# Kernel tuning notes

Hardware: AMD Instinct MI355X
Metric: run time of the kernel (lower is better)

The kernel has to match this reference:

```python
import jax, jax.numpy as jnp
import numpy as np

INTERVAL = 0.5  # voxel_size_ratio
N_RAYS = 131072
M_SAMPLES = 8388608  # ~64 samples per ray on average
ALPHA_INIT = 0.01


def setup_inputs() -> dict:
    key = jax.random.key(0)
    k1, k2, k3 = jax.random.split(key, 3)
    density = jax.random.normal(k1, (M_SAMPLES,), jnp.float32)
    rgb_feat = jax.random.normal(k2, (M_SAMPLES, 3), jnp.float32)  # raw k0 colors
    # act_shift buffer: log(1/(1-alpha_init) - 1)
    shift = jnp.array([np.log(1.0 / (1.0 - ALPHA_INIT) - 1.0)], jnp.float32)
    # sorted ray ids (samples along each ray are contiguous, near->far)
    ray_id = jnp.sort(jax.random.randint(k3, (M_SAMPLES,), 0, N_RAYS)).astype(jnp.int32)
    return {"density": density, "rgb_feat": rgb_feat, "shift": shift,
            "ray_id": ray_id, "N": N_RAYS}


def reference(density, rgb_feat, shift, ray_id, N):
    # Raw2Alpha: alpha = 1 - (1 + exp(density + shift))^(-interval)
    #          = 1 - exp(-softplus(density + shift) * interval)
    sp = jax.nn.softplus(density + shift[0])
    log1ma = -sp * INTERVAL            # log(1 - alpha), exact
    alpha = 1.0 - jnp.exp(log1ma)

    # Alphas2Weights: per-ray exclusive cumulative product of (1 - alpha)
    # done in log space with a segmented exclusive cumsum.
    seg_tot = jax.ops.segment_sum(log1ma, ray_id, num_segments=N)   # [N] log prod per ray
    seg_excl = jnp.cumsum(seg_tot) - seg_tot                        # log prod of previous rays
    within_excl = jnp.cumsum(log1ma) - log1ma - seg_excl[ray_id]    # exclusive within segment
    T = jnp.exp(within_excl)          # transmittance before each sample
    weights = alpha * T               # [M]
    alphainv_last = jnp.exp(seg_tot)  # [N] leftover transmittance per ray

    # composite colors per ray + white-ish background via alphainv_last
    rgb = jax.nn.sigmoid(rgb_feat)
    rgb_marched = jax.ops.segment_sum(weights[:, None] * rgb, ray_id, num_segments=N)
    out = rgb_marched + alphainv_last[:, None]   # [N, 3]
    return weights, alphainv_last, out
```

## Files before the change

kernel.cpp:

```cpp
#include <hip/hip_runtime.h>


__device__ __forceinline__ float fast_sigmoid(float x) {
    return __builtin_amdgcn_rcpf(1.0f + __expf(-x));
}

#define DPP_ADD(x, ctrl, rmask)                                               \
    do {                                                                      \
        int _s = __builtin_amdgcn_update_dpp(0, __float_as_int(x), (ctrl),    \
                                             (rmask), 0xf, true);             \
        (x) += __int_as_float(_s);                                            \
    } while (0)

#define DPP_MUL(x, ctrl, rmask)                                               \
    do {                                                                      \
        int _s = __builtin_amdgcn_update_dpp(0x3f800000, __float_as_int(x),   \
                                             (ctrl), (rmask), 0xf, false);    \
        (x) *= __int_as_float(_s);                                            \
    } while (0)

__device__ __forceinline__ float wave_scan_add(float x) {
    DPP_ADD(x, 0x111, 0xf);
    DPP_ADD(x, 0x112, 0xf);
    DPP_ADD(x, 0x114, 0xf);
    DPP_ADD(x, 0x118, 0xf);
    DPP_ADD(x, 0x142, 0xa);
    DPP_ADD(x, 0x143, 0xc);
    return x;
}

__device__ __forceinline__ float wave_scan_mul(float x) {
    DPP_MUL(x, 0x111, 0xf);
    DPP_MUL(x, 0x112, 0xf);
    DPP_MUL(x, 0x114, 0xf);
    DPP_MUL(x, 0x118, 0xf);
    DPP_MUL(x, 0x142, 0xa);
    DPP_MUL(x, 0x143, 0xc);
    return x;
}

__device__ __forceinline__ float bcast_lane63(float x) {
    return __int_as_float(__builtin_amdgcn_readlane(__float_as_int(x), 63));
}

__global__ __launch_bounds__(256) void seg_starts4_kernel(
    const int4* __restrict__ ray4, int M4, int M, int N,
    const int* __restrict__ ray_id, int* __restrict__ starts)
{
    const int i = blockIdx.x * blockDim.x + threadIdx.x;
    if (i >= M4) return;
    const int4 v = ray4[i];
    const int prev = (i == 0) ? -1 : ray_id[4 * i - 1];
    const int base = 4 * i;
    for (int r = prev + 1; r <= v.x; ++r) starts[r] = base;
    for (int r = v.x + 1;  r <= v.y; ++r) starts[r] = base + 1;
    for (int r = v.y + 1;  r <= v.z; ++r) starts[r] = base + 2;
    for (int r = v.z + 1;  r <= v.w; ++r) starts[r] = base + 3;
    if (i == M4 - 1) {
        int last = v.w;
        for (int j = 4 * M4; j < M; ++j) {
            const int cur = ray_id[j];
            for (int r = last + 1; r <= cur; ++r) starts[r] = j;
            last = cur;
        }
        for (int r = last + 1; r <= N; ++r) starts[r] = M;
    }
}

#define RPW 4

__global__ __launch_bounds__(256) void favor_render_kernel(
    const float* __restrict__ density,
    const float* __restrict__ rgb_feat,
    const float* __restrict__ shift,
    const int*   __restrict__ starts,
    int M, int N,
    float* __restrict__ weights,
    float* __restrict__ alphainv_last,
    float* __restrict__ out3)
{
    const int wave = (blockIdx.x * blockDim.x + threadIdx.x) >> 6;
    const int t    = threadIdx.x & 63;
    const int r0   = wave * RPW;
    if (r0 >= N) return;

    const int bv = starts[min(r0 + t, N)];
    int s[RPW + 1];
    #pragma unroll
    for (int k = 0; k <= RPW; ++k)
        s[k] = __builtin_amdgcn_readlane(bv, k);

    const float sh = shift[0];

    float pd[RPW], pr[RPW], pg[RPW], pb[RPW];
    #pragma unroll
    for (int j = 0; j < RPW; ++j) {
        const int c = max(min(s[j] + t, s[j + 1] - 1), 0);
        pd[j] = density[c];
        pr[j] = rgb_feat[3 * c + 0];
        pg[j] = rgb_feat[3 * c + 1];
        pb[j] = rgb_feat[3 * c + 2];
    }

    #pragma unroll
    for (int j = 0; j < RPW; ++j) {
        const int ray = r0 + j;
        if (ray >= N) continue;
        const int st = s[j], en = s[j + 1];

        float carryT = 1.0f;
        float a0 = 0.0f, a1 = 0.0f, a2 = 0.0f;

        {
            const bool valid = (st + t) < en;
            const float u = 1.0f + __expf(pd[j] + sh);
            const float a = __builtin_amdgcn_rsqf(u);
            const float m = valid ? a : 1.0f;
            const float S = wave_scan_mul(m);
            const float tot = bcast_lane63(S);
            const float w = S * (u * a - 1.0f);
            if (valid) {
                weights[st + t] = w;
                a0 = w * fast_sigmoid(pr[j]);
                a1 = w * fast_sigmoid(pg[j]);
                a2 = w * fast_sigmoid(pb[j]);
            }
            carryT = tot;
        }

        for (int base = st + 64; base < en; base += 64) {
            const int i = base + t;
            const bool valid = i < en;
            const int c = min(i, en - 1);
            const float d = density[c];
            const float r = rgb_feat[3 * c + 0];
            const float g = rgb_feat[3 * c + 1];
            const float b = rgb_feat[3 * c + 2];
            const float u = 1.0f + __expf(d + sh);
            const float a = __builtin_amdgcn_rsqf(u);
            const float m = valid ? a : 1.0f;
            const float S = wave_scan_mul(m);
            const float tot = bcast_lane63(S);
            const float w = carryT * S * (u * a - 1.0f);
            if (valid) {
                weights[i] = w;
                a0 += w * fast_sigmoid(r);
                a1 += w * fast_sigmoid(g);
                a2 += w * fast_sigmoid(b);
            }
            carryT *= tot;
        }

        const float t0 = bcast_lane63(wave_scan_add(a0));
        const float t1 = bcast_lane63(wave_scan_add(a1));
        const float t2 = bcast_lane63(wave_scan_add(a2));
        if (t == 0) {
            alphainv_last[ray] = carryT;
            out3[3 * ray + 0] = t0 + carryT;
            out3[3 * ray + 1] = t1 + carryT;
            out3[3 * ray + 2] = t2 + carryT;
        }
    }
}

extern "C" void kernel_launch(void* const* d_in, const int* in_sizes, int n_in,
                              void* d_out, int out_size, void* d_ws, size_t ws_size,
                              hipStream_t stream) {
    const float* density  = (const float*)d_in[0];
    const float* rgb_feat = (const float*)d_in[1];
    const float* shift    = (const float*)d_in[2];
    const int*   ray_id   = (const int*)d_in[3];

    const int M = in_sizes[0];
    const int N = (out_size - M) / 4;

    float* weights       = (float*)d_out;
    float* alphainv_last = weights + M;
    float* out3          = alphainv_last + N;

    const int block = 256;
    int* starts = (int*)d_ws;

    const int M4 = M >> 2;
    const int grid_starts = (M4 + block - 1) / block;
    seg_starts4_kernel<<<grid_starts, block, 0, stream>>>(
        (const int4*)ray_id, M4, M, N, ray_id, starts);

    const int n_waves = (N + RPW - 1) / RPW;
    const int grid_render = (n_waves * 64 + block - 1) / block;
    favor_render_kernel<<<grid_render, block, 0, stream>>>(
        density, rgb_feat, shift, starts, M, N,
        weights, alphainv_last, out3);
}
```

Baseline: 215.6 us.

## Prefetch first two 64-sample chunks for all rays and interleave per-ray scans

The render kernel now loads the first two 64-sample chunks of all four rays up front and processes chunk 0 and chunk 1 for every ray in interleaved loops. The final wave reductions are batched across rays, and launch bounds now request 4 blocks per CU. With about 64 samples per ray, most rays fit in these two chunks, so more independent memory loads are in flight before the serial scan work starts. The cost is roughly double the register use for prefetched values, and the occupancy hint may force spills or cap registers.

```diff
diff --git a/kernel.cpp b/kernel.cpp
--- a/kernel.cpp
+++ b/kernel.cpp
@@ -69,7 +69,7 @@
 
 #define RPW 4
 
-__global__ __launch_bounds__(256) void favor_render_kernel(
+__global__ __launch_bounds__(256, 4) void favor_render_kernel(
     const float* __restrict__ density,
     const float* __restrict__ rgb_feat,
     const float* __restrict__ shift,
@@ -92,43 +92,63 @@
 
     const float sh = shift[0];
 
-    float pd[RPW], pr[RPW], pg[RPW], pb[RPW];
-    #pragma unroll
-    for (int j = 0; j < RPW; ++j) {
-        const int c = max(min(s[j] + t, s[j + 1] - 1), 0);
-        pd[j] = density[c];
-        pr[j] = rgb_feat[3 * c + 0];
-        pg[j] = rgb_feat[3 * c + 1];
-        pb[j] = rgb_feat[3 * c + 2];
-    }
-
-    #pragma unroll
-    for (int j = 0; j < RPW; ++j) {
-        const int ray = r0 + j;
-        if (ray >= N) continue;
-        const int st = s[j], en = s[j + 1];
-
-        float carryT = 1.0f;
-        float a0 = 0.0f, a1 = 0.0f, a2 = 0.0f;
-
-        {
-            const bool valid = (st + t) < en;
-            const float u = 1.0f + __expf(pd[j] + sh);
-            const float a = __builtin_amdgcn_rsqf(u);
-            const float m = valid ? a : 1.0f;
-            const float S = wave_scan_mul(m);
-            const float tot = bcast_lane63(S);
-            const float w = S * (u * a - 1.0f);
-            if (valid) {
-                weights[st + t] = w;
-                a0 = w * fast_sigmoid(pr[j]);
-                a1 = w * fast_sigmoid(pg[j]);
-                a2 = w * fast_sigmoid(pb[j]);
-            }
-            carryT = tot;
-        }
-
-        for (int base = st + 64; base < en; base += 64) {
+    float d0[RPW], r0v[RPW], g0v[RPW], b0v[RPW];
+    float d1[RPW], r1v[RPW], g1v[RPW], b1v[RPW];
+    #pragma unroll
+    for (int j = 0; j < RPW; ++j) {
+        const int st = s[j], en = s[j + 1];
+        const int c0 = max(min(st + t,      en - 1), 0);
+        const int c1 = max(min(st + 64 + t, en - 1), 0);
+        d0[j]  = density[c0];
+        r0v[j] = rgb_feat[3 * c0 + 0];
+        g0v[j] = rgb_feat[3 * c0 + 1];
+        b0v[j] = rgb_feat[3 * c0 + 2];
+        d1[j]  = density[c1];
+        r1v[j] = rgb_feat[3 * c1 + 0];
+        g1v[j] = rgb_feat[3 * c1 + 1];
+        b1v[j] = rgb_feat[3 * c1 + 2];
+    }
+
+    float carryT[RPW], accR[RPW], accG[RPW], accB[RPW];
+
+    #pragma unroll
+    for (int j = 0; j < RPW; ++j) {
+        const int st = s[j], en = s[j + 1];
+        const bool valid = (st + t) < en;
+        const float u = 1.0f + __expf(d0[j] + sh);
+        const float a = __builtin_amdgcn_rsqf(u);
+        const float m = valid ? a : 1.0f;
+        const float S = wave_scan_mul(m);
+        carryT[j] = bcast_lane63(S);
+        const float w = S * (u * a - 1.0f);
+        accR[j] = valid ? w * fast_sigmoid(r0v[j]) : 0.0f;
+        accG[j] = valid ? w * fast_sigmoid(g0v[j]) : 0.0f;
+        accB[j] = valid ? w * fast_sigmoid(b0v[j]) : 0.0f;
+        if (valid) weights[st + t] = w;
+    }
+
+    #pragma unroll
+    for (int j = 0; j < RPW; ++j) {
+        const int st = s[j], en = s[j + 1];
+        const int i = st + 64 + t;
+        const bool valid = i < en;
+        const float u = 1.0f + __expf(d1[j] + sh);
+        const float a = __builtin_amdgcn_rsqf(u);
+        const float m = valid ? a : 1.0f;
+        const float S = wave_scan_mul(m);
+        const float tot = bcast_lane63(S);
+        const float w = carryT[j] * S * (u * a - 1.0f);
+        accR[j] += valid ? w * fast_sigmoid(r1v[j]) : 0.0f;
+        accG[j] += valid ? w * fast_sigmoid(g1v[j]) : 0.0f;
+        accB[j] += valid ? w * fast_sigmoid(b1v[j]) : 0.0f;
+        if (valid) weights[i] = w;
+        carryT[j] *= tot;
+    }
+
+    #pragma unroll
+    for (int j = 0; j < RPW; ++j) {
+        const int st = s[j], en = s[j + 1];
+        for (int base = st + 128; base < en; base += 64) {
             const int i = base + t;
             const bool valid = i < en;
             const int c = min(i, en - 1);
@@ -141,24 +161,35 @@
             const float m = valid ? a : 1.0f;
             const float S = wave_scan_mul(m);
             const float tot = bcast_lane63(S);
-            const float w = carryT * S * (u * a - 1.0f);
+            const float w = carryT[j] * S * (u * a - 1.0f);
             if (valid) {
                 weights[i] = w;
-                a0 += w * fast_sigmoid(r);
-                a1 += w * fast_sigmoid(g);
-                a2 += w * fast_sigmoid(b);
+                accR[j] += w * fast_sigmoid(r);
+                accG[j] += w * fast_sigmoid(g);
+                accB[j] += w * fast_sigmoid(b);
             }
-            carryT *= tot;
+            carryT[j] *= tot;
         }
-
-        const float t0 = bcast_lane63(wave_scan_add(a0));
-        const float t1 = bcast_lane63(wave_scan_add(a1));
-        const float t2 = bcast_lane63(wave_scan_add(a2));
-        if (t == 0) {
-            alphainv_last[ray] = carryT;
-            out3[3 * ray + 0] = t0 + carryT;
-            out3[3 * ray + 1] = t1 + carryT;
-            out3[3 * ray + 2] = t2 + carryT;
+    }
+
+    float tR[RPW], tG[RPW], tB[RPW];
+    #pragma unroll
+    for (int j = 0; j < RPW; ++j) {
+        tR[j] = wave_scan_add(accR[j]);
+        tG[j] = wave_scan_add(accG[j]);
+        tB[j] = wave_scan_add(accB[j]);
+    }
+    #pragma unroll
+    for (int j = 0; j < RPW; ++j) {
+        const float sR = bcast_lane63(tR[j]);
+        const float sG = bcast_lane63(tG[j]);
+        const float sB = bcast_lane63(tB[j]);
+        const int ray = r0 + j;
+        if (t == 0 && ray < N) {
+            alphainv_last[ray] = carryT[j];
+            out3[3 * ray + 0] = sR + carryT[j];
+            out3[3 * ray + 1] = sG + carryT[j];
+            out3[3 * ray + 2] = sB + carryT[j];
         }
     }
 }
```

After: 209.9 us. 2.6% less time.

## Split each wave into two half-wave rays, processing four samples per lane

Applied to the files above, without the earlier changes.

The render kernel now assigns one ray to each 32-lane half of a wave (two rays per wave) instead of looping a full wave over four rays. Each lane handles four consecutive samples with vectorized 4-wide loads of density and rgb, takes a local product, and runs a 32-lane DPP scan whose results are redistributed with ds_bpermute. The intent is to cut wasted lanes on short rays (about 64 samples each) and to reduce scan and load instruction overhead per sample. In exchange it adds unaligned vector loads, tail-case branches and a per-lane serial product, and the two halves of a wave now share one loop trip count.

```diff
diff --git a/kernel.cpp b/kernel.cpp
--- a/kernel.cpp
+++ b/kernel.cpp
@@ -4,6 +4,9 @@
 __device__ __forceinline__ float fast_sigmoid(float x) {
     return __builtin_amdgcn_rcpf(1.0f + __expf(-x));
 }
+
+struct __align__(4) f3  { float x, y, z; };
+struct __align__(4) f4s { float x, y, z, w; };
 
 #define DPP_ADD(x, ctrl, rmask)                                               \
     do {                                                                      \
@@ -19,28 +22,26 @@
         (x) *= __int_as_float(_s);                                            \
     } while (0)
 
-__device__ __forceinline__ float wave_scan_add(float x) {
+__device__ __forceinline__ float half_scan_mul(float x) {
+    DPP_MUL(x, 0x111, 0xf);
+    DPP_MUL(x, 0x112, 0xf);
+    DPP_MUL(x, 0x114, 0xf);
+    DPP_MUL(x, 0x118, 0xf);
+    DPP_MUL(x, 0x142, 0xa);
+    return x;
+}
+__device__ __forceinline__ float half_scan_add(float x) {
     DPP_ADD(x, 0x111, 0xf);
     DPP_ADD(x, 0x112, 0xf);
     DPP_ADD(x, 0x114, 0xf);
     DPP_ADD(x, 0x118, 0xf);
     DPP_ADD(x, 0x142, 0xa);
-    DPP_ADD(x, 0x143, 0xc);
     return x;
 }
 
-__device__ __forceinline__ float wave_scan_mul(float x) {
-    DPP_MUL(x, 0x111, 0xf);
-    DPP_MUL(x, 0x112, 0xf);
-    DPP_MUL(x, 0x114, 0xf);
-    DPP_MUL(x, 0x118, 0xf);
-    DPP_MUL(x, 0x142, 0xa);
-    DPP_MUL(x, 0x143, 0xc);
-    return x;
-}
-
-__device__ __forceinline__ float bcast_lane63(float x) {
-    return __int_as_float(__builtin_amdgcn_readlane(__float_as_int(x), 63));
+__device__ __forceinline__ float bperm_f(int lane, float v) {
+    return __int_as_float(
+        __builtin_amdgcn_ds_bpermute(lane * 4, __float_as_int(v)));
 }
 
 __global__ __launch_bounds__(256) void seg_starts4_kernel(
@@ -67,9 +68,9 @@
     }
 }
 
-#define RPW 4
-
-__global__ __launch_bounds__(256) void favor_render_kernel(
+#define RPW 2
+
+__global__ __launch_bounds__(256, 4) void favor_render_kernel(
     const float* __restrict__ density,
     const float* __restrict__ rgb_feat,
     const float* __restrict__ shift,
@@ -85,80 +86,105 @@
     if (r0 >= N) return;
 
     const int bv = starts[min(r0 + t, N)];
-    int s[RPW + 1];
-    #pragma unroll
-    for (int k = 0; k <= RPW; ++k)
-        s[k] = __builtin_amdgcn_readlane(bv, k);
+    const int s0 = __builtin_amdgcn_readlane(bv, 0);
+    const int s1 = __builtin_amdgcn_readlane(bv, 1);
+    const int s2 = __builtin_amdgcn_readlane(bv, 2);
+
+    const int  half = t >> 5;
+    const int  r    = t & 31;
+    const int  st   = half ? s1 : s0;
+    const int  en   = half ? s2 : s1;
+    const int  len0 = s1 - s0, len1 = s2 - s1;
 
     const float sh = shift[0];
-
-    float pd[RPW], pr[RPW], pg[RPW], pb[RPW];
-    #pragma unroll
-    for (int j = 0; j < RPW; ++j) {
-        const int c = max(min(s[j] + t, s[j + 1] - 1), 0);
-        pd[j] = density[c];
-        pr[j] = rgb_feat[3 * c + 0];
-        pg[j] = rgb_feat[3 * c + 1];
-        pb[j] = rgb_feat[3 * c + 2];
-    }
-
-    #pragma unroll
-    for (int j = 0; j < RPW; ++j) {
-        const int ray = r0 + j;
-        if (ray >= N) continue;
-        const int st = s[j], en = s[j + 1];
-
-        float carryT = 1.0f;
-        float a0 = 0.0f, a1 = 0.0f, a2 = 0.0f;
-
-        {
-            const bool valid = (st + t) < en;
-            const float u = 1.0f + __expf(pd[j] + sh);
-            const float a = __builtin_amdgcn_rsqf(u);
-            const float m = valid ? a : 1.0f;
-            const float S = wave_scan_mul(m);
-            const float tot = bcast_lane63(S);
-            const float w = S * (u * a - 1.0f);
-            if (valid) {
-                weights[st + t] = w;
-                a0 = w * fast_sigmoid(pr[j]);
-                a1 = w * fast_sigmoid(pg[j]);
-                a2 = w * fast_sigmoid(pb[j]);
-            }
-            carryT = tot;
-        }
-
-        for (int base = st + 64; base < en; base += 64) {
-            const int i = base + t;
-            const bool valid = i < en;
-            const int c = min(i, en - 1);
-            const float d = density[c];
-            const float r = rgb_feat[3 * c + 0];
-            const float g = rgb_feat[3 * c + 1];
-            const float b = rgb_feat[3 * c + 2];
-            const float u = 1.0f + __expf(d + sh);
-            const float a = __builtin_amdgcn_rsqf(u);
-            const float m = valid ? a : 1.0f;
-            const float S = wave_scan_mul(m);
-            const float tot = bcast_lane63(S);
-            const float w = carryT * S * (u * a - 1.0f);
-            if (valid) {
-                weights[i] = w;
-                a0 += w * fast_sigmoid(r);
-                a1 += w * fast_sigmoid(g);
-                a2 += w * fast_sigmoid(b);
-            }
-            carryT *= tot;
-        }
-
-        const float t0 = bcast_lane63(wave_scan_add(a0));
-        const float t1 = bcast_lane63(wave_scan_add(a1));
-        const float t2 = bcast_lane63(wave_scan_add(a2));
-        if (t == 0) {
-            alphainv_last[ray] = carryT;
-            out3[3 * ray + 0] = t0 + carryT;
-            out3[3 * ray + 1] = t1 + carryT;
-            out3[3 * ray + 2] = t2 + carryT;
+    const bool unsafe_tail = (s2 > M - 4);
+
+    float carry = 1.0f, accR = 0.0f, accG = 0.0f, accB = 0.0f;
+    int off = 0;
+
+    do {
+        const int i0 = st + off + 4 * r;
+
+        float d0, d1, d2, d3;
+        f3 c0, c1, c2, c3;
+        if (unsafe_tail) {
+            const int k0 = max(min(i0,     en - 1), 0);
+            const int k1 = max(min(i0 + 1, en - 1), 0);
+            const int k2 = max(min(i0 + 2, en - 1), 0);
+            const int k3 = max(min(i0 + 3, en - 1), 0);
+            d0 = density[k0]; d1 = density[k1];
+            d2 = density[k2]; d3 = density[k3];
+            c0 = *(const f3*)(rgb_feat + 3 * k0);
+            c1 = *(const f3*)(rgb_feat + 3 * k1);
+            c2 = *(const f3*)(rgb_feat + 3 * k2);
+            c3 = *(const f3*)(rgb_feat + 3 * k3);
+        } else {
+            const int b  = (i0 < en) ? i0 : max(en - 4, 0);
+            const f4s dv = *(const f4s*)(density + b);
+            const f4s q0 = *(const f4s*)(rgb_feat + 3 * b);
+            const f4s q1 = *(const f4s*)(rgb_feat + 3 * b + 4);
+            const f4s q2 = *(const f4s*)(rgb_feat + 3 * b + 8);
+            d0 = dv.x; d1 = dv.y; d2 = dv.z; d3 = dv.w;
+            c0.x = q0.x; c0.y = q0.y; c0.z = q0.z;
+            c1.x = q0.w; c1.y = q1.x; c1.z = q1.y;
+            c2.x = q1.z; c2.y = q1.w; c2.z = q2.x;
+            c3.x = q2.y; c3.y = q2.z; c3.z = q2.w;
+        }
+
+        const bool v0 = (i0     < en), v1 = (i0 + 1 < en);
+        const bool v2 = (i0 + 2 < en), v3 = (i0 + 3 < en);
+
+        const float u0 = 1.0f + __expf(d0 + sh);
+        const float u1 = 1.0f + __expf(d1 + sh);
+        const float u2 = 1.0f + __expf(d2 + sh);
+        const float u3 = 1.0f + __expf(d3 + sh);
+        const float a0 = v0 ? __builtin_amdgcn_rsqf(u0) : 1.0f;
+        const float a1 = v1 ? __builtin_amdgcn_rsqf(u1) : 1.0f;
+        const float a2 = v2 ? __builtin_amdgcn_rsqf(u2) : 1.0f;
+        const float a3 = v3 ? __builtin_amdgcn_rsqf(u3) : 1.0f;
+
+        const float m = (a0 * a1) * (a2 * a3);
+        const float S = half_scan_mul(m);
+        float E = bperm_f((t + 63) & 63, S);
+        E = (r == 0) ? 1.0f : E;
+        const float tot = bperm_f(t | 31, S);
+
+        float p = carry * E;
+        const float w0 = p * (1.0f - a0); p *= a0;
+        const float w1 = p * (1.0f - a1); p *= a1;
+        const float w2 = p * (1.0f - a2); p *= a2;
+        const float w3 = p * (1.0f - a3);
+
+        accR += w0 * fast_sigmoid(c0.x) + w1 * fast_sigmoid(c1.x)
+              + w2 * fast_sigmoid(c2.x) + w3 * fast_sigmoid(c3.x);
+        accG += w0 * fast_sigmoid(c0.y) + w1 * fast_sigmoid(c1.y)
+              + w2 * fast_sigmoid(c2.y) + w3 * fast_sigmoid(c3.y);
+        accB += w0 * fast_sigmoid(c0.z) + w1 * fast_sigmoid(c1.z)
+              + w2 * fast_sigmoid(c2.z) + w3 * fast_sigmoid(c3.z);
+
+        if (v3) {
+            f4s wv; wv.x = w0; wv.y = w1; wv.z = w2; wv.w = w3;
+            *(f4s*)(weights + i0) = wv;
+        } else {
+            if (v0) weights[i0]     = w0;
+            if (v1) weights[i0 + 1] = w1;
+            if (v2) weights[i0 + 2] = w2;
+        }
+
+        carry *= tot;
+        off += 128;
+    } while (len0 > off || len1 > off);
+
+    accR = half_scan_add(accR);
+    accG = half_scan_add(accG);
+    accB = half_scan_add(accB);
+    if ((t & 31) == 31) {
+        const int ray = r0 + half;
+        if (ray < N) {
+            alphainv_last[ray] = carry;
+            f3 o;
+            o.x = accR + carry; o.y = accG + carry; o.z = accB + carry;
+            *(f3*)(out3 + 3 * ray) = o;
         }
     }
 }
```

After: 214.7 us. About the same (-0.4%).
